# Performance work log

Measured on AMD Instinct MI355X. Metric: run time of the kernel, lower is better.

Reference implementation:

```python
import jax, jax.numpy as jnp
import numpy as np
from jax import lax

OVERLAP_THRESHOLD = 0.5
STUFF_AREA_LIMIT = 4096.0
CONF_THRESHOLD = 0.5
NUM_STUFF_CLASSES = 54


def setup_inputs() -> dict:
    key = jax.random.key(0)
    ks = jax.random.split(key, 5)
    N, M, H, W = 2, 100, 1024, 1024
    return {
        "scores": jax.random.uniform(ks[0], (N, M), jnp.float32),
        "classes": jax.random.randint(ks[1], (N, M), 0, 80, jnp.int32),
        "is_valid": jnp.ones((N, M), jnp.bool_),
        "boxes": jax.random.uniform(ks[2], (N, M, 4), jnp.float32),
        "masks": jax.random.normal(ks[3], (N, M, H, W), jnp.float32),
        "sem_seg": jax.random.randint(ks[4], (N, H, W), 0, NUM_STUFF_CLASSES, jnp.int32),
    }


def _combine_one(scores, classes, is_valid, boxes, masks, sem_seg):
    # scores/classes/is_valid: [M]; boxes: [M,4]; masks: [M,H,W]; sem_seg: [H,W]
    H, W = sem_seg.shape
    order = jnp.argsort(-scores)

    # --- instance segments: serial greedy merge in score order ---
    def inst_step(carry, idx):
        pano, seg_id = carry
        m = masks[idx] > 0
        area = jnp.sum(m.astype(jnp.float32))
        inter = jnp.sum((m & (pano > 0)).astype(jnp.float32))
        ratio = inter / jnp.maximum(area, 1.0)  # masks binary -> safe; area>0 gate below
        valid = (is_valid[idx]
                 & (scores[idx] > CONF_THRESHOLD)
                 & (area > 0)
                 & (ratio < OVERLAP_THRESHOLD))
        new_mask = valid & m & ~(pano > 0)
        seg_id = seg_id + 1
        pano = pano + seg_id * new_mask.astype(jnp.int32)
        info = (seg_id, jnp.bool_(True), scores[idx], classes[idx],
                idx.astype(jnp.int32), boxes[idx], valid, area)
        return (pano, seg_id), info

    init = (jnp.zeros_like(sem_seg, dtype=jnp.int32), jnp.int32(0))
    (pano, seg_id), inst_info = lax.scan(inst_step, init, order)

    # --- stuff segments: labels 1..num_stuff_classes-1 (label 0 skipped) ---
    yy = jnp.arange(H, dtype=jnp.int32)[:, None]
    xx = jnp.arange(W, dtype=jnp.int32)[None, :]
    labels = jnp.arange(1, NUM_STUFF_CLASSES, dtype=jnp.int32)

    def stuff_step(carry, lbl):
        pano, seg_id = carry
        mask = (sem_seg == lbl) & ~(pano > 0)
        area = jnp.sum(mask.astype(jnp.float32))
        valid = area > STUFF_AREA_LIMIT
        ymin = jnp.min(jnp.where(mask, yy, H))
        xmin = jnp.min(jnp.where(mask, xx, W))
        ymax = jnp.max(jnp.where(mask, yy, -1))
        xmax = jnp.max(jnp.where(mask, xx, -1))
        box = jnp.where(valid,
                        jnp.stack([ymin, xmin, ymax, xmax]).astype(jnp.float32),
                        jnp.zeros((4,), jnp.float32))
        use = mask & valid
        seg_id = seg_id + 1
        pano = pano + seg_id * use.astype(jnp.int32)
        info = (seg_id, jnp.bool_(False), jnp.float32(0.5), lbl,
                jnp.int32(0), box, valid, area)
        return (pano, seg_id), info

    (pano, _), stuff_info = lax.scan(stuff_step, (pano, seg_id), labels)

    merged = tuple(jnp.concatenate([a, b], axis=0) for a, b in zip(inst_info, stuff_info))
    # (panoptic_seg, id, isthing, score, category_id, instance_id, bbox, is_valid, area)
    return (pano,) + merged


def reference(scores, classes, is_valid, boxes, masks, sem_seg):
    return jax.vmap(_combine_one)(scores, classes, is_valid, boxes, masks, sem_seg)
```

## Files before the change

kernel.cpp:

```cpp
#include <hip/hip_runtime.h>
#include <stdint.h>

#define HWPX (1024*1024)
#define NWRD 32768
#define NBATCH 2
#define NINST 100
#define NCHUNK 13
#define NSEG 153

#define OFF_HIST  0
#define OFF_ORDER 16384
#define OFF_PRE   16640
#define OFF_GVAL  16896
#define OFF_GAREA 17152
#define OFF_SAREA 17408
#define OFF_SYMIN 17536
#define OFF_SXMIN 17664
#define OFF_SYMAX 17792
#define OFF_SXMAX 17920
#define OFF_SVAL  18048
#define OFF_CLAIM 32768
#define OFF_BITS  131072

#define O_PANO  0
#define O_ID    2097152
#define O_ISTH  (O_ID    + NBATCH*NSEG)
#define O_SCORE (O_ISTH  + NBATCH*NSEG)
#define O_CAT   (O_SCORE + NBATCH*NSEG)
#define O_INST  (O_CAT   + NBATCH*NSEG)
#define O_BBOX  (O_INST  + NBATCH*NSEG)
#define O_VALID (O_BBOX  + NBATCH*NSEG*4)
#define O_AREA  (O_VALID + NBATCH*NSEG)

__global__ void k_init(int* __restrict__ ws) {
    int i = blockIdx.x * 256 + threadIdx.x;
    if (i >= 98304) return;
    int v = 0;
    if ((i >= OFF_SYMIN && i < OFF_SYMIN + 108) ||
        (i >= OFF_SXMIN && i < OFF_SXMIN + 108)) v = 2147483647;
    if ((i >= OFF_SYMAX && i < OFF_SYMAX + 108) ||
        (i >= OFF_SXMAX && i < OFF_SXMAX + 108)) v = (int)0x80000000;
    ws[i] = v;
}

__global__ void k_sort(const float* __restrict__ scores, int* __restrict__ ws) {
    int tid = threadIdx.x;
    if (tid >= NBATCH * NINST) return;
    int n = tid / NINST, i = tid % NINST;
    float si = scores[n * NINST + i];
    int rank = 0;
    for (int j = 0; j < NINST; j++) {
        float sj = scores[n * NINST + j];
        rank += (sj > si) || (sj == si && j < i);
    }
    ws[OFF_ORDER + n * NINST + rank] = i;
    ws[OFF_PRE   + n * NINST + rank] = (si > 0.5f) ? 1 : 0;
}

__launch_bounds__(256)
__global__ void k_chunk(const float* __restrict__ masks, int* __restrict__ ws, int c) {
    __shared__ int s_hist[512];
    __shared__ int s_acc;
    __shared__ int s_order[8];
    const int tid = threadIdx.x;
    const int gw  = blockIdx.x * 256 + tid;
    const int n   = gw >> 15;
    const int w   = gw & 32767;

    s_hist[tid] = 0; s_hist[tid + 256] = 0;
    const int kcur = min(8, NINST - c * 8);
    if (tid < kcur) s_order[tid] = ws[OFF_ORDER + n * NINST + c * 8 + tid];

    if (c > 0) {
        if (tid < 64) {
            const int* hg = ws + OFF_HIST + ((c - 1) * 2 + n) * 512;
            int h[8];
            #pragma unroll
            for (int k = 0; k < 8; k++) h[k] = hg[tid + 64 * k];
            int accMask = 0, myArea = 0;
            for (int j = 0; j < 8; j++) {
                int a = 0, it = 0;
                #pragma unroll
                for (int k = 0; k < 8; k++) {
                    int bin = tid + 64 * k;
                    if ((bin >> j) & 1) {
                        a += h[k];
                        if ((bin >> 8) | (bin & accMask)) it += h[k];
                    }
                }
                #pragma unroll
                for (int off = 32; off >= 1; off >>= 1) {
                    a  += __shfl_xor(a,  off, 64);
                    it += __shfl_xor(it, off, 64);
                }
                int pv = ws[OFF_PRE + n * NINST + (c - 1) * 8 + j];
                int valid = pv && (a > 0) &&
                            (((float)it / fmaxf((float)a, 1.0f)) < 0.5f);
                if (valid) accMask |= (1 << j);
                if (tid == j) myArea = a;
            }
            if (tid == 0) s_acc = accMask;
            if ((blockIdx.x & 127) == 0 && tid < 8) {
                ws[OFF_GVAL  + n * NINST + (c - 1) * 8 + tid] = (accMask >> tid) & 1;
                ws[OFF_GAREA + n * NINST + (c - 1) * 8 + tid] = myArea;
            }
        }
    } else if (tid == 0) {
        s_acc = 0;
    }
    __syncthreads();

    uint32_t* claimed = (uint32_t*)(ws + OFF_CLAIM);
    uint32_t* bitmaps = (uint32_t*)(ws + OFF_BITS);

    uint32_t cw = claimed[n * NWRD + w];
    const int accPrev = s_acc;
    if (c > 0 && accPrev) {
        #pragma unroll
        for (int j = 0; j < 8; j++)
            if ((accPrev >> j) & 1)
                cw |= bitmaps[(size_t)(n * NINST + (c - 1) * 8 + j) * NWRD + w];
    }
    claimed[n * NWRD + w] = cw;

    uint32_t wd[8];
    #pragma unroll
    for (int j = 0; j < 8; j++) wd[j] = 0;
    for (int j = 0; j < kcur; j++) {
        const float* mp = masks + (size_t)(n * NINST + s_order[j]) * HWPX + (size_t)w * 32;
        uint32_t bits = 0;
        #pragma unroll
        for (int q = 0; q < 8; q++) {
            float4 v = ((const float4*)mp)[q];
            bits |= (uint32_t)(v.x > 0.f) << (4 * q + 0);
            bits |= (uint32_t)(v.y > 0.f) << (4 * q + 1);
            bits |= (uint32_t)(v.z > 0.f) << (4 * q + 2);
            bits |= (uint32_t)(v.w > 0.f) << (4 * q + 3);
        }
        wd[j] = bits;
        bitmaps[(size_t)(n * NINST + c * 8 + j) * NWRD + w] = bits;
    }

    #pragma unroll
    for (int p = 0; p < 32; p++) {
        int pat = (int)((cw >> p) & 1u) << 8;
        #pragma unroll
        for (int j = 0; j < 8; j++) pat |= (int)((wd[j] >> p) & 1u) << j;
        atomicAdd(&s_hist[pat], 1);
    }
    __syncthreads();
    int* hg = ws + OFF_HIST + (c * 2 + n) * 512;
    if (s_hist[tid])       atomicAdd(&hg[tid],       s_hist[tid]);
    if (s_hist[tid + 256]) atomicAdd(&hg[tid + 256], s_hist[tid + 256]);
}

__global__ void k_decide_info(const float* __restrict__ scores, const int* __restrict__ classes,
                              const float* __restrict__ boxes, int* __restrict__ ws,
                              float* __restrict__ out) {
    int tid = threadIdx.x;
    int wv = tid >> 6, lane = tid & 63;
    if (wv < 2) {
        int n = wv;
        const int* hg = ws + OFF_HIST + (12 * 2 + n) * 512;
        int h[8];
        #pragma unroll
        for (int k = 0; k < 8; k++) h[k] = hg[lane + 64 * k];
        int accMask = 0, myArea = 0;
        for (int j = 0; j < 4; j++) {
            int a = 0, it = 0;
            #pragma unroll
            for (int k = 0; k < 8; k++) {
                int bin = lane + 64 * k;
                if ((bin >> j) & 1) {
                    a += h[k];
                    if ((bin >> 8) | (bin & accMask)) it += h[k];
                }
            }
            #pragma unroll
            for (int off = 32; off >= 1; off >>= 1) {
                a  += __shfl_xor(a,  off, 64);
                it += __shfl_xor(it, off, 64);
            }
            int pv = ws[OFF_PRE + n * NINST + 96 + j];
            int valid = pv && (a > 0) && (((float)it / fmaxf((float)a, 1.0f)) < 0.5f);
            if (valid) accMask |= (1 << j);
            if (lane == j) myArea = a;
        }
        if (lane < 4) {
            ws[OFF_GVAL  + n * NINST + 96 + lane] = (accMask >> lane) & 1;
            ws[OFF_GAREA + n * NINST + 96 + lane] = myArea;
        }
    }
    __syncthreads();
    if (tid < NBATCH * NINST) {
        int n = tid / NINST, t = tid % NINST;
        int m  = ws[OFF_ORDER + n * NINST + t];
        int gv = ws[OFF_GVAL  + n * NINST + t];
        int ga = ws[OFF_GAREA + n * NINST + t];
        int slot = n * NSEG + t;
        out[O_ID    + slot] = (float)(t + 1);
        out[O_ISTH  + slot] = 1.0f;
        out[O_SCORE + slot] = scores[n * NINST + m];
        out[O_CAT   + slot] = (float)classes[n * NINST + m];
        out[O_INST  + slot] = (float)m;
        out[O_VALID + slot] = (float)gv;
        out[O_AREA  + slot] = (float)ga;
        #pragma unroll
        for (int q = 0; q < 4; q++)
            out[O_BBOX + slot * 4 + q] = boxes[(n * NINST + m) * 4 + q];
    }
}

__launch_bounds__(256)
__global__ void k_stuff_reduce(const int* __restrict__ sem, int* __restrict__ ws) {
    __shared__ int larea[54], lymin[54], lxmin[54], lymax[54], lxmax[54];
    __shared__ int s_v12[4];
    const int tid = threadIdx.x;
    const int gw  = blockIdx.x * 256 + tid;
    const int n   = gw >> 15;
    const int w   = gw & 32767;
    if (tid < 54) {
        larea[tid] = 0;
        lymin[tid] = 2147483647; lxmin[tid] = 2147483647;
        lymax[tid] = (int)0x80000000; lxmax[tid] = (int)0x80000000;
    }
    if (tid < 4) s_v12[tid] = ws[OFF_GVAL + n * NINST + 96 + tid];
    __syncthreads();

    uint32_t* claimed = (uint32_t*)(ws + OFF_CLAIM);
    const uint32_t* bitmaps = (const uint32_t*)(ws + OFF_BITS);
    uint32_t cw = claimed[n * NWRD + w];
    #pragma unroll
    for (int j = 0; j < 4; j++)
        if (s_v12[j]) cw |= bitmaps[(size_t)(n * NINST + 96 + j) * NWRD + w];
    claimed[n * NWRD + w] = cw;

    uint32_t un = ~cw;
    if (un) {
        int y = (w * 32) >> 10;
        const int* sp = sem + (size_t)n * HWPX + (size_t)w * 32;
        for (int p = 0; p < 32; p++) {
            if ((un >> p) & 1u) {
                int lbl = sp[p];
                if (lbl > 0 && lbl < 54) {
                    int x = (w * 32 + p) & 1023;
                    atomicAdd(&larea[lbl], 1);
                    atomicMin(&lymin[lbl], y); atomicMax(&lymax[lbl], y);
                    atomicMin(&lxmin[lbl], x); atomicMax(&lxmax[lbl], x);
                }
            }
        }
    }
    __syncthreads();
    if (tid < 54 && larea[tid]) {
        atomicAdd(ws + OFF_SAREA + n * 54 + tid, larea[tid]);
        atomicMin(ws + OFF_SYMIN + n * 54 + tid, lymin[tid]);
        atomicMin(ws + OFF_SXMIN + n * 54 + tid, lxmin[tid]);
        atomicMax(ws + OFF_SYMAX + n * 54 + tid, lymax[tid]);
        atomicMax(ws + OFF_SXMAX + n * 54 + tid, lxmax[tid]);
    }
}

__global__ void k_stuff_info(int* __restrict__ ws, float* __restrict__ out) {
    int tid = threadIdx.x;
    if (tid >= NBATCH * 53) return;
    int n = tid / 53, lbl = tid % 53 + 1;
    int area  = ws[OFF_SAREA + n * 54 + lbl];
    int valid = area > 4096;
    ws[OFF_SVAL + n * 54 + lbl] = valid;
    int slot = n * NSEG + 99 + lbl;
    out[O_ID    + slot] = (float)(100 + lbl);
    out[O_ISTH  + slot] = 0.0f;
    out[O_SCORE + slot] = 0.5f;
    out[O_CAT   + slot] = (float)lbl;
    out[O_INST  + slot] = 0.0f;
    out[O_VALID + slot] = (float)valid;
    out[O_AREA  + slot] = (float)area;
    float b0 = 0.f, b1 = 0.f, b2 = 0.f, b3 = 0.f;
    if (valid) {
        b0 = (float)ws[OFF_SYMIN + n * 54 + lbl];
        b1 = (float)ws[OFF_SXMIN + n * 54 + lbl];
        b2 = (float)ws[OFF_SYMAX + n * 54 + lbl];
        b3 = (float)ws[OFF_SXMAX + n * 54 + lbl];
    }
    out[O_BBOX + slot * 4 + 0] = b0;
    out[O_BBOX + slot * 4 + 1] = b1;
    out[O_BBOX + slot * 4 + 2] = b2;
    out[O_BBOX + slot * 4 + 3] = b3;
}

__launch_bounds__(256)
__global__ void k_finalize(const int* __restrict__ sem, const int* __restrict__ ws,
                           float* __restrict__ out) {
    __shared__ int accT[100];
    __shared__ int s_nacc;
    __shared__ char s_sv[54];
    const int tid = threadIdx.x;
    const int gw  = blockIdx.x * 256 + tid;
    const int n   = gw >> 15;
    const int w   = gw & 32767;
    if (tid == 0) {
        int k = 0;
        for (int t = 0; t < NINST; t++)
            if (ws[OFF_GVAL + n * NINST + t]) accT[k++] = t;
        s_nacc = k;
    }
    if (tid < 54) s_sv[tid] = (char)ws[OFF_SVAL + n * 54 + tid];
    __syncthreads();

    const uint32_t* claimed = (const uint32_t*)(ws + OFF_CLAIM);
    const uint32_t* bitmaps = (const uint32_t*)(ws + OFF_BITS);
    uint32_t cw = claimed[n * NWRD + w];
    const int* sp = sem + (size_t)n * HWPX + (size_t)w * 32;

    float val[32];
    #pragma unroll
    for (int q = 0; q < 8; q++) {
        int4 s4 = ((const int4*)sp)[q];
        const int pb = 4 * q;
        val[pb + 0] = (!((cw >> (pb + 0)) & 1u) && s4.x > 0 && s4.x < 54 && s_sv[s4.x]) ? (float)(100 + s4.x) : 0.f;
        val[pb + 1] = (!((cw >> (pb + 1)) & 1u) && s4.y > 0 && s4.y < 54 && s_sv[s4.y]) ? (float)(100 + s4.y) : 0.f;
        val[pb + 2] = (!((cw >> (pb + 2)) & 1u) && s4.z > 0 && s4.z < 54 && s_sv[s4.z]) ? (float)(100 + s4.z) : 0.f;
        val[pb + 3] = (!((cw >> (pb + 3)) & 1u) && s4.w > 0 && s4.w < 54 && s_sv[s4.w]) ? (float)(100 + s4.w) : 0.f;
    }

    uint32_t remaining = cw;
    const int nacc = s_nacc;
    for (int k = 0; k < nacc; k++) {
        if (__ballot(remaining != 0u) == 0ULL) break;
        if (remaining) {
            int t = accT[k];
            uint32_t bits = bitmaps[(size_t)(n * NINST + t) * NWRD + w] & remaining;
            if (bits) {
                remaining &= ~bits;
                float fv = (float)(t + 1);
                #pragma unroll
                for (int p = 0; p < 32; p++)
                    if ((bits >> p) & 1u) val[p] = fv;
            }
        }
    }

    float4* op = (float4*)(out + O_PANO + (size_t)n * HWPX + (size_t)w * 32);
    #pragma unroll
    for (int q = 0; q < 8; q++)
        op[q] = make_float4(val[4 * q], val[4 * q + 1], val[4 * q + 2], val[4 * q + 3]);
}

extern "C" void kernel_launch(void* const* d_in, const int* in_sizes, int n_in,
                              void* d_out, int out_size, void* d_ws, size_t ws_size,
                              hipStream_t stream) {
    const float* scores  = (const float*)d_in[0];
    const int*   classes = (const int*)d_in[1];
    const float* boxes   = (const float*)d_in[3];
    const float* masks   = (const float*)d_in[4];
    const int*   sem     = (const int*)d_in[5];
    int*   ws  = (int*)d_ws;
    float* out = (float*)d_out;

    k_init <<<dim3(384), dim3(256), 0, stream>>>(ws);
    k_sort <<<dim3(1),   dim3(256), 0, stream>>>(scores, ws);
    for (int c = 0; c < NCHUNK; c++)
        k_chunk<<<dim3(256), dim3(256), 0, stream>>>(masks, ws, c);
    k_decide_info<<<dim3(1),   dim3(256), 0, stream>>>(scores, classes, boxes, ws, out);
    k_stuff_reduce<<<dim3(256), dim3(256), 0, stream>>>(sem, ws);
    k_stuff_info <<<dim3(1),   dim3(128), 0, stream>>>(ws, out);
    k_finalize   <<<dim3(256), dim3(256), 0, stream>>>(sem, ws, out);
}
```

Measured before the change: 1.204 ms.

## Process instances in chunks of ten with byte-granular bitmaps and replicated histograms

Each thread now handles 8 pixels (one byte of bitmap) instead of 32, and the grid grows from 256 to 1024 blocks. Instances are grouped ten per chunk, so there are 10 chunk passes instead of 13, using 2048-bin shared histograms. Global histograms and stuff reductions are spread over 8 copies to reduce atomic contention. The per-chunk decision moves into a separate small kernel, which adds a launch per chunk in exchange for fewer chunks and more parallelism in the bandwidth-bound mask pass.

```diff
diff --git a/kernel.cpp b/kernel.cpp
--- a/kernel.cpp
+++ b/kernel.cpp
@@ -1,26 +1,31 @@
 #include <hip/hip_runtime.h>
 #include <stdint.h>
+#include <limits.h>
 
 #define HWPX (1024*1024)
-#define NWRD 32768
+#define NBYTE 131072
 #define NBATCH 2
 #define NINST 100
-#define NCHUNK 13
+#define CHN 10
+#define NCH 10
+#define NBIN 2048
+#define NCOPY 8
 #define NSEG 153
 
 #define OFF_HIST  0
-#define OFF_ORDER 16384
-#define OFF_PRE   16640
-#define OFF_GVAL  16896
-#define OFF_GAREA 17152
-#define OFF_SAREA 17408
-#define OFF_SYMIN 17536
-#define OFF_SXMIN 17664
-#define OFF_SYMAX 17792
-#define OFF_SXMAX 17920
-#define OFF_SVAL  18048
-#define OFF_CLAIM 32768
-#define OFF_BITS  131072
+#define OFF_ORDER 327680
+#define OFF_PRE   327880
+#define OFF_GVAL  328080
+#define OFF_GAREA 328280
+#define OFF_SAREA 328480
+#define OFF_SYMIN 329344
+#define OFF_SXMIN 330208
+#define OFF_SYMAX 331072
+#define OFF_SXMAX 331936
+#define OFF_SVAL  332800
+#define OFF_CLAIM 333824
+#define OFF_BITS  399360
+#define INIT_END  399360
 
 #define O_PANO  0
 #define O_ID    2097152
@@ -34,12 +39,9 @@
 
 __global__ void k_init(int* __restrict__ ws) {
     int i = blockIdx.x * 256 + threadIdx.x;
-    if (i >= 98304) return;
     int v = 0;
-    if ((i >= OFF_SYMIN && i < OFF_SYMIN + 108) ||
-        (i >= OFF_SXMIN && i < OFF_SXMIN + 108)) v = 2147483647;
-    if ((i >= OFF_SYMAX && i < OFF_SYMAX + 108) ||
-        (i >= OFF_SXMAX && i < OFF_SXMAX + 108)) v = (int)0x80000000;
+    if (i >= OFF_SYMIN && i < OFF_SYMAX) v = INT_MAX;
+    else if (i >= OFF_SYMAX && i < OFF_SVAL) v = INT_MIN;
     ws[i] = v;
 }
 
@@ -57,193 +59,175 @@
     ws[OFF_PRE   + n * NINST + rank] = (si > 0.5f) ? 1 : 0;
 }
 
-__launch_bounds__(256)
+__launch_bounds__(256, 4)
 __global__ void k_chunk(const float* __restrict__ masks, int* __restrict__ ws, int c) {
-    __shared__ int s_hist[512];
+    __shared__ int s_hist[NBIN];
+    __shared__ int s_ord[CHN];
     __shared__ int s_acc;
-    __shared__ int s_order[8];
     const int tid = threadIdx.x;
-    const int gw  = blockIdx.x * 256 + tid;
-    const int n   = gw >> 15;
-    const int w   = gw & 32767;
-
-    s_hist[tid] = 0; s_hist[tid + 256] = 0;
-    const int kcur = min(8, NINST - c * 8);
-    if (tid < kcur) s_order[tid] = ws[OFF_ORDER + n * NINST + c * 8 + tid];
-
-    if (c > 0) {
-        if (tid < 64) {
-            const int* hg = ws + OFF_HIST + ((c - 1) * 2 + n) * 512;
-            int h[8];
-            #pragma unroll
-            for (int k = 0; k < 8; k++) h[k] = hg[tid + 64 * k];
-            int accMask = 0, myArea = 0;
-            for (int j = 0; j < 8; j++) {
-                int a = 0, it = 0;
-                #pragma unroll
-                for (int k = 0; k < 8; k++) {
-                    int bin = tid + 64 * k;
-                    if ((bin >> j) & 1) {
-                        a += h[k];
-                        if ((bin >> 8) | (bin & accMask)) it += h[k];
-                    }
-                }
-                #pragma unroll
-                for (int off = 32; off >= 1; off >>= 1) {
-                    a  += __shfl_xor(a,  off, 64);
-                    it += __shfl_xor(it, off, 64);
-                }
-                int pv = ws[OFF_PRE + n * NINST + (c - 1) * 8 + j];
-                int valid = pv && (a > 0) &&
-                            (((float)it / fmaxf((float)a, 1.0f)) < 0.5f);
-                if (valid) accMask |= (1 << j);
-                if (tid == j) myArea = a;
+    const int gb  = blockIdx.x * 256 + tid;
+    const int n   = gb >> 17;
+    const int b   = gb & (NBYTE - 1);
+
+    #pragma unroll
+    for (int k = 0; k < NBIN / 256; k++) s_hist[tid + 256 * k] = 0;
+    if (tid < CHN) s_ord[tid] = ws[OFF_ORDER + n * NINST + c * CHN + tid];
+    if (tid == 0) {
+        int am = 0;
+        if (c > 0)
+            for (int j = 0; j < CHN; j++)
+                am |= ws[OFF_GVAL + n * NINST + (c - 1) * CHN + j] << j;
+        s_acc = am;
+    }
+    __syncthreads();
+
+    uint8_t* claimed = (uint8_t*)(ws + OFF_CLAIM);
+    uint8_t* bitmaps = (uint8_t*)(ws + OFF_BITS);
+
+    uint32_t cw = claimed[n * NBYTE + b];
+    const int acc = s_acc;
+    if (acc) {
+        #pragma unroll
+        for (int j = 0; j < CHN; j++)
+            if ((acc >> j) & 1)
+                cw |= bitmaps[(size_t)(n * NINST + (c - 1) * CHN + j) * NBYTE + b];
+    }
+    claimed[n * NBYTE + b] = (uint8_t)cw;
+
+    uint32_t wd[CHN];
+    #pragma unroll
+    for (int j = 0; j < CHN; j++) {
+        const float4* mp = (const float4*)(masks + ((size_t)(n * NINST + s_ord[j]) << 20)) + (size_t)b * 2;
+        float4 v0 = mp[0], v1 = mp[1];
+        uint32_t bits =  (uint32_t)(v0.x > 0.f)
+                      | ((uint32_t)(v0.y > 0.f) << 1)
+                      | ((uint32_t)(v0.z > 0.f) << 2)
+                      | ((uint32_t)(v0.w > 0.f) << 3)
+                      | ((uint32_t)(v1.x > 0.f) << 4)
+                      | ((uint32_t)(v1.y > 0.f) << 5)
+                      | ((uint32_t)(v1.z > 0.f) << 6)
+                      | ((uint32_t)(v1.w > 0.f) << 7);
+        wd[j] = bits;
+        bitmaps[(size_t)(n * NINST + c * CHN + j) * NBYTE + b] = (uint8_t)bits;
+    }
+
+    #pragma unroll
+    for (int p = 0; p < 8; p++) {
+        int pat = (int)((cw >> p) & 1u) << CHN;
+        #pragma unroll
+        for (int j = 0; j < CHN; j++) pat |= (int)((wd[j] >> p) & 1u) << j;
+        atomicAdd(&s_hist[pat], 1);
+    }
+    __syncthreads();
+
+    int* hg = ws + OFF_HIST + ((c * 2 + n) * NCOPY + (blockIdx.x & (NCOPY - 1))) * NBIN;
+    #pragma unroll
+    for (int k = 0; k < NBIN / 256; k++) {
+        int v = s_hist[tid + 256 * k];
+        if (v) atomicAdd(&hg[tid + 256 * k], v);
+    }
+}
+
+__global__ void k_decide(int* __restrict__ ws, int c) {
+    const int n = blockIdx.x;
+    const int lane = threadIdx.x;
+    const int* hb = ws + OFF_HIST + (c * 2 + n) * NCOPY * NBIN;
+    int h[32];
+    #pragma unroll
+    for (int k = 0; k < 32; k++) h[k] = 0;
+    #pragma unroll
+    for (int cp = 0; cp < NCOPY; cp++) {
+        const int4* p4 = (const int4*)(hb + cp * NBIN + lane * 32);
+        #pragma unroll
+        for (int q = 0; q < 8; q++) {
+            int4 v = p4[q];
+            h[q * 4 + 0] += v.x; h[q * 4 + 1] += v.y;
+            h[q * 4 + 2] += v.z; h[q * 4 + 3] += v.w;
+        }
+    }
+    int accMask = 0, myArea = 0;
+    for (int j = 0; j < CHN; j++) {
+        int a = 0, it = 0;
+        #pragma unroll
+        for (int k = 0; k < 32; k++) {
+            int bin = lane * 32 + k;
+            if ((bin >> j) & 1) {
+                a += h[k];
+                if ((bin >> CHN) | (bin & accMask)) it += h[k];
             }
-            if (tid == 0) s_acc = accMask;
-            if ((blockIdx.x & 127) == 0 && tid < 8) {
-                ws[OFF_GVAL  + n * NINST + (c - 1) * 8 + tid] = (accMask >> tid) & 1;
-                ws[OFF_GAREA + n * NINST + (c - 1) * 8 + tid] = myArea;
-            }
-        }
-    } else if (tid == 0) {
-        s_acc = 0;
-    }
-    __syncthreads();
-
-    uint32_t* claimed = (uint32_t*)(ws + OFF_CLAIM);
-    uint32_t* bitmaps = (uint32_t*)(ws + OFF_BITS);
-
-    uint32_t cw = claimed[n * NWRD + w];
-    const int accPrev = s_acc;
-    if (c > 0 && accPrev) {
-        #pragma unroll
-        for (int j = 0; j < 8; j++)
-            if ((accPrev >> j) & 1)
-                cw |= bitmaps[(size_t)(n * NINST + (c - 1) * 8 + j) * NWRD + w];
-    }
-    claimed[n * NWRD + w] = cw;
-
-    uint32_t wd[8];
-    #pragma unroll
-    for (int j = 0; j < 8; j++) wd[j] = 0;
-    for (int j = 0; j < kcur; j++) {
-        const float* mp = masks + (size_t)(n * NINST + s_order[j]) * HWPX + (size_t)w * 32;
-        uint32_t bits = 0;
-        #pragma unroll
-        for (int q = 0; q < 8; q++) {
-            float4 v = ((const float4*)mp)[q];
-            bits |= (uint32_t)(v.x > 0.f) << (4 * q + 0);
-            bits |= (uint32_t)(v.y > 0.f) << (4 * q + 1);
-            bits |= (uint32_t)(v.z > 0.f) << (4 * q + 2);
-            bits |= (uint32_t)(v.w > 0.f) << (4 * q + 3);
-        }
-        wd[j] = bits;
-        bitmaps[(size_t)(n * NINST + c * 8 + j) * NWRD + w] = bits;
-    }
-
-    #pragma unroll
-    for (int p = 0; p < 32; p++) {
-        int pat = (int)((cw >> p) & 1u) << 8;
-        #pragma unroll
-        for (int j = 0; j < 8; j++) pat |= (int)((wd[j] >> p) & 1u) << j;
-        atomicAdd(&s_hist[pat], 1);
-    }
-    __syncthreads();
-    int* hg = ws + OFF_HIST + (c * 2 + n) * 512;
-    if (s_hist[tid])       atomicAdd(&hg[tid],       s_hist[tid]);
-    if (s_hist[tid + 256]) atomicAdd(&hg[tid + 256], s_hist[tid + 256]);
-}
-
-__global__ void k_decide_info(const float* __restrict__ scores, const int* __restrict__ classes,
-                              const float* __restrict__ boxes, int* __restrict__ ws,
-                              float* __restrict__ out) {
+        }
+        #pragma unroll
+        for (int off = 32; off >= 1; off >>= 1) {
+            a  += __shfl_xor(a,  off, 64);
+            it += __shfl_xor(it, off, 64);
+        }
+        int pv = ws[OFF_PRE + n * NINST + c * CHN + j];
+        int valid = pv && (a > 0) && (((float)it / fmaxf((float)a, 1.0f)) < 0.5f);
+        accMask |= valid << j;
+        if (lane == j) myArea = a;
+    }
+    if (lane < CHN) {
+        ws[OFF_GVAL  + n * NINST + c * CHN + lane] = (accMask >> lane) & 1;
+        ws[OFF_GAREA + n * NINST + c * CHN + lane] = myArea;
+    }
+}
+
+__global__ void k_info(const float* __restrict__ scores, const int* __restrict__ classes,
+                       const float* __restrict__ boxes, const int* __restrict__ ws,
+                       float* __restrict__ out) {
     int tid = threadIdx.x;
-    int wv = tid >> 6, lane = tid & 63;
-    if (wv < 2) {
-        int n = wv;
-        const int* hg = ws + OFF_HIST + (12 * 2 + n) * 512;
-        int h[8];
-        #pragma unroll
-        for (int k = 0; k < 8; k++) h[k] = hg[lane + 64 * k];
-        int accMask = 0, myArea = 0;
-        for (int j = 0; j < 4; j++) {
-            int a = 0, it = 0;
-            #pragma unroll
-            for (int k = 0; k < 8; k++) {
-                int bin = lane + 64 * k;
-                if ((bin >> j) & 1) {
-                    a += h[k];
-                    if ((bin >> 8) | (bin & accMask)) it += h[k];
-                }
-            }
-            #pragma unroll
-            for (int off = 32; off >= 1; off >>= 1) {
-                a  += __shfl_xor(a,  off, 64);
-                it += __shfl_xor(it, off, 64);
-            }
-            int pv = ws[OFF_PRE + n * NINST + 96 + j];
-            int valid = pv && (a > 0) && (((float)it / fmaxf((float)a, 1.0f)) < 0.5f);
-            if (valid) accMask |= (1 << j);
-            if (lane == j) myArea = a;
-        }
-        if (lane < 4) {
-            ws[OFF_GVAL  + n * NINST + 96 + lane] = (accMask >> lane) & 1;
-            ws[OFF_GAREA + n * NINST + 96 + lane] = myArea;
-        }
-    }
-    __syncthreads();
-    if (tid < NBATCH * NINST) {
-        int n = tid / NINST, t = tid % NINST;
-        int m  = ws[OFF_ORDER + n * NINST + t];
-        int gv = ws[OFF_GVAL  + n * NINST + t];
-        int ga = ws[OFF_GAREA + n * NINST + t];
-        int slot = n * NSEG + t;
-        out[O_ID    + slot] = (float)(t + 1);
-        out[O_ISTH  + slot] = 1.0f;
-        out[O_SCORE + slot] = scores[n * NINST + m];
-        out[O_CAT   + slot] = (float)classes[n * NINST + m];
-        out[O_INST  + slot] = (float)m;
-        out[O_VALID + slot] = (float)gv;
-        out[O_AREA  + slot] = (float)ga;
-        #pragma unroll
-        for (int q = 0; q < 4; q++)
-            out[O_BBOX + slot * 4 + q] = boxes[(n * NINST + m) * 4 + q];
-    }
+    if (tid >= NBATCH * NINST) return;
+    int n = tid / NINST, t = tid % NINST;
+    int m  = ws[OFF_ORDER + n * NINST + t];
+    int slot = n * NSEG + t;
+    out[O_ID    + slot] = (float)(t + 1);
+    out[O_ISTH  + slot] = 1.0f;
+    out[O_SCORE + slot] = scores[n * NINST + m];
+    out[O_CAT   + slot] = (float)classes[n * NINST + m];
+    out[O_INST  + slot] = (float)m;
+    out[O_VALID + slot] = (float)ws[OFF_GVAL  + n * NINST + t];
+    out[O_AREA  + slot] = (float)ws[OFF_GAREA + n * NINST + t];
+    #pragma unroll
+    for (int q = 0; q < 4; q++)
+        out[O_BBOX + slot * 4 + q] = boxes[(n * NINST + m) * 4 + q];
 }
 
 __launch_bounds__(256)
 __global__ void k_stuff_reduce(const int* __restrict__ sem, int* __restrict__ ws) {
     __shared__ int larea[54], lymin[54], lxmin[54], lymax[54], lxmax[54];
-    __shared__ int s_v12[4];
+    __shared__ int s_v[CHN];
     const int tid = threadIdx.x;
-    const int gw  = blockIdx.x * 256 + tid;
-    const int n   = gw >> 15;
-    const int w   = gw & 32767;
+    const int gb  = blockIdx.x * 256 + tid;
+    const int n   = gb >> 17;
+    const int b   = gb & (NBYTE - 1);
     if (tid < 54) {
         larea[tid] = 0;
-        lymin[tid] = 2147483647; lxmin[tid] = 2147483647;
-        lymax[tid] = (int)0x80000000; lxmax[tid] = (int)0x80000000;
-    }
-    if (tid < 4) s_v12[tid] = ws[OFF_GVAL + n * NINST + 96 + tid];
-    __syncthreads();
-
-    uint32_t* claimed = (uint32_t*)(ws + OFF_CLAIM);
-    const uint32_t* bitmaps = (const uint32_t*)(ws + OFF_BITS);
-    uint32_t cw = claimed[n * NWRD + w];
-    #pragma unroll
-    for (int j = 0; j < 4; j++)
-        if (s_v12[j]) cw |= bitmaps[(size_t)(n * NINST + 96 + j) * NWRD + w];
-    claimed[n * NWRD + w] = cw;
-
-    uint32_t un = ~cw;
+        lymin[tid] = INT_MAX; lxmin[tid] = INT_MAX;
+        lymax[tid] = INT_MIN; lxmax[tid] = INT_MIN;
+    }
+    if (tid < CHN) s_v[tid] = ws[OFF_GVAL + n * NINST + (NCH - 1) * CHN + tid];
+    __syncthreads();
+
+    uint8_t* claimed = (uint8_t*)(ws + OFF_CLAIM);
+    const uint8_t* bitmaps = (const uint8_t*)(ws + OFF_BITS);
+    uint32_t cw = claimed[n * NBYTE + b];
+    #pragma unroll
+    for (int j = 0; j < CHN; j++)
+        if (s_v[j]) cw |= bitmaps[(size_t)(n * NINST + (NCH - 1) * CHN + j) * NBYTE + b];
+    claimed[n * NBYTE + b] = (uint8_t)cw;
+
+    uint32_t un = ~cw & 0xffu;
+    const int* sp = sem + ((size_t)n << 20) + (size_t)b * 8;
+    int4 s0 = ((const int4*)sp)[0], s1 = ((const int4*)sp)[1];
+    int sl[8] = {s0.x, s0.y, s0.z, s0.w, s1.x, s1.y, s1.z, s1.w};
     if (un) {
-        int y = (w * 32) >> 10;
-        const int* sp = sem + (size_t)n * HWPX + (size_t)w * 32;
-        for (int p = 0; p < 32; p++) {
+        int y = b >> 7;
+        #pragma unroll
+        for (int p = 0; p < 8; p++) {
             if ((un >> p) & 1u) {
-                int lbl = sp[p];
+                int lbl = sl[p];
                 if (lbl > 0 && lbl < 54) {
-                    int x = (w * 32 + p) & 1023;
+                    int x = (b * 8 + p) & 1023;
                     atomicAdd(&larea[lbl], 1);
                     atomicMin(&lymin[lbl], y); atomicMax(&lymax[lbl], y);
                     atomicMin(&lxmin[lbl], x); atomicMax(&lxmax[lbl], x);
@@ -253,11 +237,12 @@
     }
     __syncthreads();
     if (tid < 54 && larea[tid]) {
-        atomicAdd(ws + OFF_SAREA + n * 54 + tid, larea[tid]);
-        atomicMin(ws + OFF_SYMIN + n * 54 + tid, lymin[tid]);
-        atomicMin(ws + OFF_SXMIN + n * 54 + tid, lxmin[tid]);
-        atomicMax(ws + OFF_SYMAX + n * 54 + tid, lymax[tid]);
-        atomicMax(ws + OFF_SXMAX + n * 54 + tid, lxmax[tid]);
+        int base = (n * NCOPY + (blockIdx.x & (NCOPY - 1))) * 54 + tid;
+        atomicAdd(ws + OFF_SAREA + base, larea[tid]);
+        atomicMin(ws + OFF_SYMIN + base, lymin[tid]);
+        atomicMin(ws + OFF_SXMIN + base, lxmin[tid]);
+        atomicMax(ws + OFF_SYMAX + base, lymax[tid]);
+        atomicMax(ws + OFF_SXMAX + base, lxmax[tid]);
     }
 }
 
@@ -265,7 +250,15 @@
     int tid = threadIdx.x;
     if (tid >= NBATCH * 53) return;
     int n = tid / 53, lbl = tid % 53 + 1;
-    int area  = ws[OFF_SAREA + n * 54 + lbl];
+    int area = 0, ymin = INT_MAX, xmin = INT_MAX, ymax = INT_MIN, xmax = INT_MIN;
+    for (int cp = 0; cp < NCOPY; cp++) {
+        int base = (n * NCOPY + cp) * 54 + lbl;
+        area += ws[OFF_SAREA + base];
+        ymin = min(ymin, ws[OFF_SYMIN + base]);
+        xmin = min(xmin, ws[OFF_SXMIN + base]);
+        ymax = max(ymax, ws[OFF_SYMAX + base]);
+        xmax = max(xmax, ws[OFF_SXMAX + base]);
+    }
     int valid = area > 4096;
     ws[OFF_SVAL + n * 54 + lbl] = valid;
     int slot = n * NSEG + 99 + lbl;
@@ -276,29 +269,22 @@
     out[O_INST  + slot] = 0.0f;
     out[O_VALID + slot] = (float)valid;
     out[O_AREA  + slot] = (float)area;
-    float b0 = 0.f, b1 = 0.f, b2 = 0.f, b3 = 0.f;
-    if (valid) {
-        b0 = (float)ws[OFF_SYMIN + n * 54 + lbl];
-        b1 = (float)ws[OFF_SXMIN + n * 54 + lbl];
-        b2 = (float)ws[OFF_SYMAX + n * 54 + lbl];
-        b3 = (float)ws[OFF_SXMAX + n * 54 + lbl];
-    }
-    out[O_BBOX + slot * 4 + 0] = b0;
-    out[O_BBOX + slot * 4 + 1] = b1;
-    out[O_BBOX + slot * 4 + 2] = b2;
-    out[O_BBOX + slot * 4 + 3] = b3;
+    out[O_BBOX + slot * 4 + 0] = valid ? (float)ymin : 0.f;
+    out[O_BBOX + slot * 4 + 1] = valid ? (float)xmin : 0.f;
+    out[O_BBOX + slot * 4 + 2] = valid ? (float)ymax : 0.f;
+    out[O_BBOX + slot * 4 + 3] = valid ? (float)xmax : 0.f;
 }
 
 __launch_bounds__(256)
 __global__ void k_finalize(const int* __restrict__ sem, const int* __restrict__ ws,
                            float* __restrict__ out) {
-    __shared__ int accT[100];
+    __shared__ int accT[NINST];
     __shared__ int s_nacc;
     __shared__ char s_sv[54];
     const int tid = threadIdx.x;
-    const int gw  = blockIdx.x * 256 + tid;
-    const int n   = gw >> 15;
-    const int w   = gw & 32767;
+    const int gb  = blockIdx.x * 256 + tid;
+    const int n   = gb >> 17;
+    const int b   = gb & (NBYTE - 1);
     if (tid == 0) {
         int k = 0;
         for (int t = 0; t < NINST; t++)
@@ -308,20 +294,17 @@
     if (tid < 54) s_sv[tid] = (char)ws[OFF_SVAL + n * 54 + tid];
     __syncthreads();
 
-    const uint32_t* claimed = (const uint32_t*)(ws + OFF_CLAIM);
-    const uint32_t* bitmaps = (const uint32_t*)(ws + OFF_BITS);
-    uint32_t cw = claimed[n * NWRD + w];
-    const int* sp = sem + (size_t)n * HWPX + (size_t)w * 32;
-
-    float val[32];
-    #pragma unroll
-    for (int q = 0; q < 8; q++) {
-        int4 s4 = ((const int4*)sp)[q];
-        const int pb = 4 * q;
-        val[pb + 0] = (!((cw >> (pb + 0)) & 1u) && s4.x > 0 && s4.x < 54 && s_sv[s4.x]) ? (float)(100 + s4.x) : 0.f;
-        val[pb + 1] = (!((cw >> (pb + 1)) & 1u) && s4.y > 0 && s4.y < 54 && s_sv[s4.y]) ? (float)(100 + s4.y) : 0.f;
-        val[pb + 2] = (!((cw >> (pb + 2)) & 1u) && s4.z > 0 && s4.z < 54 && s_sv[s4.z]) ? (float)(100 + s4.z) : 0.f;
-        val[pb + 3] = (!((cw >> (pb + 3)) & 1u) && s4.w > 0 && s4.w < 54 && s_sv[s4.w]) ? (float)(100 + s4.w) : 0.f;
+    const uint8_t* claimed = (const uint8_t*)(ws + OFF_CLAIM);
+    const uint8_t* bitmaps = (const uint8_t*)(ws + OFF_BITS);
+    uint32_t cw = claimed[n * NBYTE + b];
+    const int* sp = sem + ((size_t)n << 20) + (size_t)b * 8;
+    int4 s0 = ((const int4*)sp)[0], s1 = ((const int4*)sp)[1];
+    int sl[8] = {s0.x, s0.y, s0.z, s0.w, s1.x, s1.y, s1.z, s1.w};
+    float val[8];
+    #pragma unroll
+    for (int p = 0; p < 8; p++) {
+        int l = sl[p];
+        val[p] = (!((cw >> p) & 1u) && l > 0 && l < 54 && s_sv[l]) ? (float)(100 + l) : 0.f;
     }
 
     uint32_t remaining = cw;
@@ -330,21 +313,20 @@
         if (__ballot(remaining != 0u) == 0ULL) break;
         if (remaining) {
             int t = accT[k];
-            uint32_t bits = bitmaps[(size_t)(n * NINST + t) * NWRD + w] & remaining;
+            uint32_t bits = bitmaps[(size_t)(n * NINST + t) * NBYTE + b] & remaining;
             if (bits) {
                 remaining &= ~bits;
                 float fv = (float)(t + 1);
                 #pragma unroll
-                for (int p = 0; p < 32; p++)
+                for (int p = 0; p < 8; p++)
                     if ((bits >> p) & 1u) val[p] = fv;
             }
         }
     }
 
-    float4* op = (float4*)(out + O_PANO + (size_t)n * HWPX + (size_t)w * 32);
-    #pragma unroll
-    for (int q = 0; q < 8; q++)
-        op[q] = make_float4(val[4 * q], val[4 * q + 1], val[4 * q + 2], val[4 * q + 3]);
+    float4* op = (float4*)(out + O_PANO + ((size_t)n << 20) + (size_t)b * 8);
+    op[0] = make_float4(val[0], val[1], val[2], val[3]);
+    op[1] = make_float4(val[4], val[5], val[6], val[7]);
 }
 
 extern "C" void kernel_launch(void* const* d_in, const int* in_sizes, int n_in,
@@ -358,12 +340,14 @@
     int*   ws  = (int*)d_ws;
     float* out = (float*)d_out;
 
-    k_init <<<dim3(384), dim3(256), 0, stream>>>(ws);
-    k_sort <<<dim3(1),   dim3(256), 0, stream>>>(scores, ws);
-    for (int c = 0; c < NCHUNK; c++)
-        k_chunk<<<dim3(256), dim3(256), 0, stream>>>(masks, ws, c);
-    k_decide_info<<<dim3(1),   dim3(256), 0, stream>>>(scores, classes, boxes, ws, out);
-    k_stuff_reduce<<<dim3(256), dim3(256), 0, stream>>>(sem, ws);
-    k_stuff_info <<<dim3(1),   dim3(128), 0, stream>>>(ws, out);
-    k_finalize   <<<dim3(256), dim3(256), 0, stream>>>(sem, ws, out);
-}
+    k_init<<<dim3(INIT_END / 256), dim3(256), 0, stream>>>(ws);
+    k_sort<<<dim3(1), dim3(256), 0, stream>>>(scores, ws);
+    for (int c = 0; c < NCH; c++) {
+        k_chunk <<<dim3(1024), dim3(256), 0, stream>>>(masks, ws, c);
+        k_decide<<<dim3(2),    dim3(64),  0, stream>>>(ws, c);
+    }
+    k_info        <<<dim3(1),    dim3(256), 0, stream>>>(scores, classes, boxes, ws, out);
+    k_stuff_reduce<<<dim3(1024), dim3(256), 0, stream>>>(sem, ws);
+    k_stuff_info  <<<dim3(1),    dim3(128), 0, stream>>>(ws, out);
+    k_finalize    <<<dim3(1024), dim3(256), 0, stream>>>(sem, ws, out);
+}
```

Result: slower. 1.284 ms (+6.6%).
